# Performance work log

Measured on AMD Instinct MI355X. Metric: run time of the kernel, lower is better.

## Reference

```python
import jax, jax.numpy as jnp
import numpy as np

TOKENS, HIDDEN, FFN = 4096, 4096, 14336
SCALE = 0.02  # keep activations in a sane range


def setup_inputs() -> dict:
    key = jax.random.key(0)
    k1, k2, k3, k4 = jax.random.split(key, 4)
    x = jax.random.normal(k1, (TOKENS, HIDDEN), dtype=jnp.float32)
    expert_w1 = jax.random.normal(k2, (FFN, HIDDEN), dtype=jnp.float32) * SCALE
    expert_v1 = jax.random.normal(k3, (FFN, HIDDEN), dtype=jnp.float32) * SCALE
    expert_w2 = jax.random.normal(k4, (FFN, HIDDEN), dtype=jnp.float32) * SCALE
    return {"x": x, "expert_w1": expert_w1, "expert_v1": expert_v1, "expert_w2": expert_w2}


def reference(x, expert_w1, expert_v1, expert_w2):
    # gate/up projections: [T, H] @ [H, F] -> [T, F]
    gate = jnp.einsum('th,fh->tf', x, expert_w1)
    up = jnp.einsum('th,fh->tf', x, expert_v1)
    inter = jax.nn.silu(gate) * up            # fused SwiGLU intermediate [T, F]
    down = jnp.einsum('tf,fh->th', inter, expert_w2)  # [T, H]
    return down
```

## Files before the change

kernel.cpp:

```cpp
#include <hip/hip_runtime.h>
#include <hip/hip_bf16.h>
#include <stdint.h>

#define TOKENS 4096
#define HIDDEN 4096
#define FFN    14336

typedef __attribute__((ext_vector_type(8))) short bf16x8;
typedef __attribute__((ext_vector_type(4))) float f32x4;
typedef __attribute__((ext_vector_type(8))) unsigned short u16x8;

typedef __attribute__((address_space(3))) void lds_void_t;
typedef const __attribute__((address_space(1))) void gbl_void_t;

static __device__ __forceinline__ unsigned short f2b(float f) {
  union { float f; unsigned int u; } v; v.f = f;
  unsigned int u = v.u;
  return (unsigned short)((u + 0x7FFFu + ((u >> 16) & 1u)) >> 16);
}
static __device__ __forceinline__ float b2f(unsigned short b) {
  union { unsigned int u; float f; } v; v.u = ((unsigned int)b) << 16;
  return v.f;
}

__global__ void cvt_kernel(const float* __restrict__ in, unsigned short* __restrict__ out, long n) {
  long idx = (long)blockIdx.x * blockDim.x + threadIdx.x;
  long stride = (long)gridDim.x * blockDim.x;
  for (long i = idx * 4; i < n; i += stride * 4) {
    const float4 v = *reinterpret_cast<const float4*>(in + i);
    ushort4 o;
    o.x = f2b(v.x); o.y = f2b(v.y); o.z = f2b(v.z); o.w = f2b(v.w);
    *reinterpret_cast<ushort4*>(out + i) = o;
  }
}

__global__ void transpose_cvt_kernel(const float* __restrict__ in, unsigned short* __restrict__ out) {
  __shared__ float tile[64][65];
  const int f0 = blockIdx.x * 64;
  const int h0 = blockIdx.y * 64;
  const int t = threadIdx.x;
  const int rcol = (t & 15) * 4;
  const int rrow = t >> 4;
#pragma unroll
  for (int it = 0; it < 4; ++it) {
    int r = rrow + it * 16;
    const float4 v = *reinterpret_cast<const float4*>(in + (long)(f0 + r) * HIDDEN + h0 + rcol);
    tile[r][rcol] = v.x; tile[r][rcol + 1] = v.y; tile[r][rcol + 2] = v.z; tile[r][rcol + 3] = v.w;
  }
  __syncthreads();
  const int wrow = t >> 2;
  const int wc = (t & 3) * 16;
  u16x8 lo, hi;
#pragma unroll
  for (int j = 0; j < 8; ++j) lo[j] = f2b(tile[wc + j][wrow]);
#pragma unroll
  for (int j = 0; j < 8; ++j) hi[j] = f2b(tile[wc + 8 + j][wrow]);
  u16x8* dst = reinterpret_cast<u16x8*>(out + (long)(h0 + wrow) * FFN + f0 + wc);
  dst[0] = lo; dst[1] = hi;
}

#define MFMA16(a, b, c) __builtin_amdgcn_mfma_f32_16x16x32_bf16((a), (b), (c), 0, 0, 0)
#define SBAR()  __builtin_amdgcn_s_barrier()
#define SCHED0() __builtin_amdgcn_sched_barrier(0)

__global__ __launch_bounds__(512, 2)
void gateup256b_kernel(const unsigned short* __restrict__ X,
                       const unsigned short* __restrict__ W1,
                       const unsigned short* __restrict__ V1,
                       unsigned short* __restrict__ Inter) {
  __shared__ unsigned short sh[65536];
  const int tid = threadIdx.x, lane = tid & 63, wid = tid >> 6;
  const int wm = wid >> 2, wn = wid & 3;
  const int bm = blockIdx.x & 15;
  const int bn = blockIdx.x >> 4;
  const int sr = tid >> 3;
  const int scb = (((tid & 7) ^ (sr & 7)) << 4);
  const int l15 = lane & 15;
  const int cb0 = (((lane >> 4) * 16) ^ ((lane & 7) << 4));
  const int cb1 = ((64 + (lane >> 4) * 16) ^ ((lane & 7) << 4));

  const unsigned short* Ap = X  + (long)(bm * 256) * HIDDEN;
  const unsigned short* Wp = W1 + (long)(bn * 128) * HIDDEN;
  const unsigned short* Vp = V1 + (long)(bn * 128) * HIDDEN;

  f32x4 acc[8][4] = {};

  auto STAGE = [&](int kind, int h, int buf, int t) {
    const unsigned short* src;
    if (kind == 0) src = Ap + (long)(h * 128 + sr) * HIDDEN + t * 64 + (scb >> 1);
    else           src = (h ? Vp : Wp) + (long)sr * HIDDEN + t * 64 + (scb >> 1);
    unsigned short* dst = sh + buf * 32768 + kind * 16384 + h * 8192 + tid * 8;
    __builtin_amdgcn_global_load_lds((gbl_void_t*)src, (lds_void_t*)dst, 16, 0, 0);
    __builtin_amdgcn_global_load_lds((gbl_void_t*)(src + 64L * HIDDEN), (lds_void_t*)(dst + 4096), 16, 0, 0);
  };
  auto LDA8 = [&](bf16x8* a, int buf, int cb) {
    const char* base = (const char*)sh + buf * 65536 + wm * 16384 + l15 * 128 + cb;
#pragma unroll
    for (int m = 0; m < 8; ++m) a[m] = *(const bf16x8*)(base + m * 2048);
  };
  auto LDB2 = [&](bf16x8* b, int buf, int cb, int np) {
    const char* base = (const char*)sh + buf * 65536 + 32768 + (wn >> 1) * 16384 +
                       ((wn & 1) * 64 + l15) * 128 + cb;
    b[2 * np]     = *(const bf16x8*)(base + (2 * np) * 2048);
    b[2 * np + 1] = *(const bf16x8*)(base + (2 * np + 1) * 2048);
  };

  STAGE(0, 0, 0, 0); STAGE(0, 1, 0, 0); STAGE(1, 0, 0, 0); STAGE(1, 1, 0, 0);

  bf16x8 a[8], b[4];
  const int NT = HIDDEN / 64;
  for (int t = 0; t < NT; ++t) {
    const int cur = t & 1, nxt = cur ^ 1;
    const bool pre = (t + 1 < NT);
    if (pre) { STAGE(1, 0, nxt, t + 1); STAGE(1, 1, nxt, t + 1);
               asm volatile("s_waitcnt vmcnt(4)" ::: "memory"); }
    else     { asm volatile("s_waitcnt vmcnt(0)" ::: "memory"); }
    SBAR(); SCHED0();
    LDA8(a, cur, cb0); LDB2(b, cur, cb0, 0);
    __builtin_amdgcn_s_setprio(1);
#pragma unroll
    for (int m = 0; m < 8; ++m) {
      acc[m][0] = MFMA16(a[m], b[0], acc[m][0]);
      acc[m][1] = MFMA16(a[m], b[1], acc[m][1]);
    }
    __builtin_amdgcn_s_setprio(0);
    SCHED0(); SBAR();
    LDB2(b, cur, cb0, 1);
    if (pre) { STAGE(0, 0, nxt, t + 1); STAGE(0, 1, nxt, t + 1); }
    SCHED0(); SBAR();
    __builtin_amdgcn_s_setprio(1);
#pragma unroll
    for (int m = 0; m < 8; ++m) {
      acc[m][2] = MFMA16(a[m], b[2], acc[m][2]);
      acc[m][3] = MFMA16(a[m], b[3], acc[m][3]);
    }
    __builtin_amdgcn_s_setprio(0);
    SCHED0(); SBAR();
    LDA8(a, cur, cb1); LDB2(b, cur, cb1, 0);
    SCHED0(); SBAR();
    __builtin_amdgcn_s_setprio(1);
#pragma unroll
    for (int m = 0; m < 8; ++m) {
      acc[m][0] = MFMA16(a[m], b[0], acc[m][0]);
      acc[m][1] = MFMA16(a[m], b[1], acc[m][1]);
    }
    __builtin_amdgcn_s_setprio(0);
    SCHED0(); SBAR();
    LDB2(b, cur, cb1, 1);
    SCHED0(); SBAR();
    __builtin_amdgcn_s_setprio(1);
#pragma unroll
    for (int m = 0; m < 8; ++m) {
      acc[m][2] = MFMA16(a[m], b[2], acc[m][2]);
      acc[m][3] = MFMA16(a[m], b[3], acc[m][3]);
    }
    __builtin_amdgcn_s_setprio(0);
    SCHED0(); SBAR();
  }
  __syncthreads();
  if (wn >= 2) {
#pragma unroll
    for (int m = 0; m < 8; ++m)
#pragma unroll
      for (int n = 0; n < 4; ++n) {
        ushort4 p;
        p.x = f2b(acc[m][n][0]); p.y = f2b(acc[m][n][1]);
        p.z = f2b(acc[m][n][2]); p.w = f2b(acc[m][n][3]);
        const int idx = ((((wm * 2 + (wn & 1)) * 8 + m) * 4 + n) * 64 + lane) * 4;
        *reinterpret_cast<ushort4*>(&sh[idx]) = p;
      }
  }
  __syncthreads();
  if (wn < 2) {
    const int r0 = (lane >> 4) * 4;
#pragma unroll
    for (int m = 0; m < 8; ++m)
#pragma unroll
      for (int n = 0; n < 4; ++n) {
        const int idx = ((((wm * 2 + wn) * 8 + m) * 4 + n) * 64 + lane) * 4;
        const ushort4 p = *reinterpret_cast<const ushort4*>(&sh[idx]);
        const float uu[4] = { b2f(p.x), b2f(p.y), b2f(p.z), b2f(p.w) };
        const int row = bm * 256 + wm * 128 + m * 16 + r0;
        const int col = bn * 128 + wn * 64 + n * 16 + l15;
#pragma unroll
        for (int r = 0; r < 4; ++r) {
          const float g = acc[m][n][r];
          const float s = g / (1.0f + __expf(-g));
          Inter[(long)(row + r) * FFN + col] = f2b(s * uu[r]);
        }
      }
  }
}

__global__ __launch_bounds__(512, 2)
void down256_kernel(const unsigned short* __restrict__ Inter,
                    const unsigned short* __restrict__ W2t,
                    float* __restrict__ Out) {
  __shared__ unsigned short sh[65536];
  const int tid = threadIdx.x, lane = tid & 63, wid = tid >> 6;
  const int wm = wid >> 2, wn = wid & 3;
  const int bm = blockIdx.x & 15;
  const int bn = blockIdx.x >> 4;
  const int sr = tid >> 3;
  const int scb = (((tid & 7) ^ (sr & 7)) << 4);
  const int l15 = lane & 15;
  const int cb0 = (((lane >> 4) * 16) ^ ((lane & 7) << 4));
  const int cb1 = ((64 + (lane >> 4) * 16) ^ ((lane & 7) << 4));

  const unsigned short* Ap = Inter + (long)(bm * 256) * FFN;
  const unsigned short* Bp = W2t + (long)(bn * 256) * FFN;

  f32x4 acc[8][4] = {};

  auto STAGE = [&](int kind, int h, int buf, int t) {
    const unsigned short* src = (kind ? Bp : Ap) + (long)(h * 128 + sr) * FFN + t * 64 + (scb >> 1);
    unsigned short* dst = sh + buf * 32768 + kind * 16384 + h * 8192 + tid * 8;
    __builtin_amdgcn_global_load_lds((gbl_void_t*)src, (lds_void_t*)dst, 16, 0, 0);
    __builtin_amdgcn_global_load_lds((gbl_void_t*)(src + 64L * FFN), (lds_void_t*)(dst + 4096), 16, 0, 0);
  };
  auto LDA8 = [&](bf16x8* a, int buf, int cb) {
    const char* base = (const char*)sh + buf * 65536 + wm * 16384 + l15 * 128 + cb;
#pragma unroll
    for (int m = 0; m < 8; ++m) a[m] = *(const bf16x8*)(base + m * 2048);
  };
  auto LDB2 = [&](bf16x8* b, int buf, int cb, int np) {
    const char* base = (const char*)sh + buf * 65536 + 32768 + (wn >> 1) * 16384 +
                       ((wn & 1) * 64 + l15) * 128 + cb;
    b[2 * np]     = *(const bf16x8*)(base + (2 * np) * 2048);
    b[2 * np + 1] = *(const bf16x8*)(base + (2 * np + 1) * 2048);
  };

  STAGE(0, 0, 0, 0); STAGE(0, 1, 0, 0); STAGE(1, 0, 0, 0); STAGE(1, 1, 0, 0);

  bf16x8 a[8], b[4];
  const int NT = FFN / 64;
  for (int t = 0; t < NT; ++t) {
    const int cur = t & 1, nxt = cur ^ 1;
    const bool pre = (t + 1 < NT);
    if (pre) { STAGE(1, 0, nxt, t + 1); STAGE(1, 1, nxt, t + 1);
               asm volatile("s_waitcnt vmcnt(4)" ::: "memory"); }
    else     { asm volatile("s_waitcnt vmcnt(0)" ::: "memory"); }
    SBAR(); SCHED0();
    LDA8(a, cur, cb0); LDB2(b, cur, cb0, 0);
    __builtin_amdgcn_s_setprio(1);
#pragma unroll
    for (int m = 0; m < 8; ++m) {
      acc[m][0] = MFMA16(a[m], b[0], acc[m][0]);
      acc[m][1] = MFMA16(a[m], b[1], acc[m][1]);
    }
    __builtin_amdgcn_s_setprio(0);
    SCHED0(); SBAR();
    LDB2(b, cur, cb0, 1);
    if (pre) { STAGE(0, 0, nxt, t + 1); STAGE(0, 1, nxt, t + 1); }
    SCHED0(); SBAR();
    __builtin_amdgcn_s_setprio(1);
#pragma unroll
    for (int m = 0; m < 8; ++m) {
      acc[m][2] = MFMA16(a[m], b[2], acc[m][2]);
      acc[m][3] = MFMA16(a[m], b[3], acc[m][3]);
    }
    __builtin_amdgcn_s_setprio(0);
    SCHED0(); SBAR();
    LDA8(a, cur, cb1); LDB2(b, cur, cb1, 0);
    SCHED0(); SBAR();
    __builtin_amdgcn_s_setprio(1);
#pragma unroll
    for (int m = 0; m < 8; ++m) {
      acc[m][0] = MFMA16(a[m], b[0], acc[m][0]);
      acc[m][1] = MFMA16(a[m], b[1], acc[m][1]);
    }
    __builtin_amdgcn_s_setprio(0);
    SCHED0(); SBAR();
    LDB2(b, cur, cb1, 1);
    SCHED0(); SBAR();
    __builtin_amdgcn_s_setprio(1);
#pragma unroll
    for (int m = 0; m < 8; ++m) {
      acc[m][2] = MFMA16(a[m], b[2], acc[m][2]);
      acc[m][3] = MFMA16(a[m], b[3], acc[m][3]);
    }
    __builtin_amdgcn_s_setprio(0);
    SCHED0(); SBAR();
  }
  const int r0 = (lane >> 4) * 4;
#pragma unroll
  for (int m = 0; m < 8; ++m)
#pragma unroll
    for (int n = 0; n < 4; ++n)
#pragma unroll
      for (int r = 0; r < 4; ++r) {
        const int row = bm * 256 + wm * 128 + m * 16 + r0 + r;
        const int col = bn * 256 + wn * 64 + n * 16 + l15;
        Out[(long)row * HIDDEN + col] = acc[m][n][r];
      }
}

__device__ __forceinline__ void stage_tile_128(const unsigned short* __restrict__ g, long ldk,
                                               unsigned short* lds, int wave, int lane) {
#pragma unroll
  for (int it = 0; it < 2; ++it) {
    const int row = (it * 4 + wave) * 16 + (lane >> 2);
    const int kcol = (lane & 3) * 8;
    const unsigned short* src = g + (long)row * ldk + kcol;
    unsigned short* dst = lds + row * 32 + kcol;
    __builtin_amdgcn_global_load_lds((gbl_void_t*)src, (lds_void_t*)dst, 16, 0, 0);
  }
}

__global__ __launch_bounds__(256, 2)
void down_nt_kernel(const unsigned short* __restrict__ Inter,
                    const float* __restrict__ W2,
                    float* __restrict__ Out) {
  __shared__ unsigned short As[128 * 32];
  __shared__ unsigned short Bs[128 * 32];
  const int t = threadIdx.x;
  const int lane = t & 63;
  const int wave = t >> 6;
  const int bm = blockIdx.x & 31;
  const int bn = blockIdx.x >> 5;
  const int wm = (wave >> 1) * 64;
  const int wn = (wave & 1) * 64;
  const unsigned short* gA = Inter + (long)(bm * 128) * FFN;

  f32x4 acc[4][4] = {};
  const int fr = lane & 15;
  const int kg = (lane >> 4) * 8;
  const int p = lane & 15;
  const int h0 = wave * 32 + (lane >> 4) * 8;
  const float* gB = W2 + bn * 128 + h0;

  for (int kt = 0; kt < FFN; kt += 32) {
    __syncthreads();
    stage_tile_128(gA + kt, FFN, As, wave, lane);
    const float* r0p = gB + (long)(kt + 2 * p) * HIDDEN;
    const float* r1p = r0p + HIDDEN;
    const float4 a0 = *reinterpret_cast<const float4*>(r0p);
    const float4 a1 = *reinterpret_cast<const float4*>(r0p + 4);
    const float4 b0 = *reinterpret_cast<const float4*>(r1p);
    const float4 b1 = *reinterpret_cast<const float4*>(r1p + 4);
    unsigned short lo[8], hi[8];
    lo[0] = f2b(a0.x); lo[1] = f2b(a0.y); lo[2] = f2b(a0.z); lo[3] = f2b(a0.w);
    lo[4] = f2b(a1.x); lo[5] = f2b(a1.y); lo[6] = f2b(a1.z); lo[7] = f2b(a1.w);
    hi[0] = f2b(b0.x); hi[1] = f2b(b0.y); hi[2] = f2b(b0.z); hi[3] = f2b(b0.w);
    hi[4] = f2b(b1.x); hi[5] = f2b(b1.y); hi[6] = f2b(b1.z); hi[7] = f2b(b1.w);
#pragma unroll
    for (int j = 0; j < 8; ++j) {
      const unsigned int pack = (unsigned int)lo[j] | ((unsigned int)hi[j] << 16);
      *reinterpret_cast<unsigned int*>(&Bs[(h0 + j) * 32 + 2 * p]) = pack;
    }
    __syncthreads();
    bf16x8 a[4], b[4];
#pragma unroll
    for (int m = 0; m < 4; ++m)
      a[m] = *reinterpret_cast<const bf16x8*>(&As[(wm + m * 16 + fr) * 32 + kg]);
#pragma unroll
    for (int n = 0; n < 4; ++n)
      b[n] = *reinterpret_cast<const bf16x8*>(&Bs[(wn + n * 16 + fr) * 32 + kg]);
#pragma unroll
    for (int m = 0; m < 4; ++m)
#pragma unroll
      for (int n = 0; n < 4; ++n)
        acc[m][n] = MFMA16(a[m], b[n], acc[m][n]);
  }
  const int r0 = (lane >> 4) * 4;
#pragma unroll
  for (int m = 0; m < 4; ++m)
#pragma unroll
    for (int n = 0; n < 4; ++n)
#pragma unroll
      for (int r = 0; r < 4; ++r) {
        const int row = bm * 128 + wm + m * 16 + r0 + r;
        const int col = bn * 128 + wn + n * 16 + fr;
        Out[(long)row * HIDDEN + col] = acc[m][n][r];
      }
}

extern "C" void kernel_launch(void* const* d_in, const int* in_sizes, int n_in,
                              void* d_out, int out_size, void* d_ws, size_t ws_size,
                              hipStream_t stream) {
  const float* x  = (const float*)d_in[0];
  const float* w1 = (const float*)d_in[1];
  const float* v1 = (const float*)d_in[2];
  const float* w2 = (const float*)d_in[3];
  float* out = (float*)d_out;

  const size_t REQ_SMALL = 385875968UL;
  const size_t REQ_FULL  = 503316480UL;
  if (ws_size < REQ_SMALL) return;
  const bool full = (ws_size >= REQ_FULL);
  char* ws = (char*)d_ws;
  unsigned short* xb     = (unsigned short*)(ws);
  unsigned short* w1b    = (unsigned short*)(ws + 33554432L);
  unsigned short* v1b    = (unsigned short*)(ws + 150994944L);
  unsigned short* interb = (unsigned short*)(ws + 268435456L);
  unsigned short* w2tb   = (unsigned short*)(ws + 385875968L);

  hipLaunchKernelGGL(cvt_kernel, dim3(2048), dim3(256), 0, stream, x,  xb,  (long)TOKENS * HIDDEN);
  hipLaunchKernelGGL(cvt_kernel, dim3(2048), dim3(256), 0, stream, w1, w1b, (long)FFN * HIDDEN);
  hipLaunchKernelGGL(cvt_kernel, dim3(2048), dim3(256), 0, stream, v1, v1b, (long)FFN * HIDDEN);
  if (full)
    hipLaunchKernelGGL(transpose_cvt_kernel, dim3(FFN / 64, HIDDEN / 64), dim3(256), 0, stream, w2, w2tb);
  hipLaunchKernelGGL(gateup256b_kernel, dim3((TOKENS / 256) * (FFN / 128)), dim3(512), 0, stream,
                     xb, w1b, v1b, interb);
  if (full)
    hipLaunchKernelGGL(down256_kernel, dim3((TOKENS / 256) * (HIDDEN / 256)), dim3(512), 0, stream,
                       interb, w2tb, out);
  else
    hipLaunchKernelGGL(down_nt_kernel, dim3((TOKENS / 128) * (HIDDEN / 128)), dim3(256), 0, stream,
                       interb, w2, out);
}
```

Baseline: 1.475 ms.

## Split gate/up into two 256x256 GEMMs with SwiGLU fused into gate epilogue

Adds a templated 256x256-tile bf16 GEMM kernel whose epilogue can write bf16, write fp32, or apply SiLU(gate)*up by reading a stored up tensor. When the workspace is large enough, the fused gate/up kernel is replaced by two GEMM launches: the up projection writes a bf16 buffer, then the gate projection consumes it in its epilogue. The down projection now uses the same template, and the fp32-W2 fallback path is removed, so a larger minimum workspace is required. The aim is a uniform, simpler main loop per GEMM, at the cost of an extra round trip of the full T x F up intermediate through memory.

```diff
diff --git a/kernel.cpp b/kernel.cpp
--- a/kernel.cpp
+++ b/kernel.cpp
@@ -62,6 +62,120 @@
 #define MFMA16(a, b, c) __builtin_amdgcn_mfma_f32_16x16x32_bf16((a), (b), (c), 0, 0, 0)
 #define SBAR()  __builtin_amdgcn_s_barrier()
 #define SCHED0() __builtin_amdgcn_sched_barrier(0)
+
+template <int LDK, int NT, int LDN, int EPI>
+__global__ __launch_bounds__(512, 2)
+void gemm256_kernel(const unsigned short* __restrict__ A,
+                    const unsigned short* __restrict__ B,
+                    void* __restrict__ OutV,
+                    const unsigned short* __restrict__ Up) {
+  __shared__ unsigned short sh[65536];
+  const int tid = threadIdx.x, lane = tid & 63, wid = tid >> 6;
+  const int wm = wid >> 2, wn = wid & 3;
+  const int bm = blockIdx.x & 15;
+  const int bn = blockIdx.x >> 4;
+  const int sr = tid >> 3;
+  const int scb = (((tid & 7) ^ (sr & 7)) << 4);
+  const int l15 = lane & 15;
+  const int cb0 = (((lane >> 4) * 16) ^ ((lane & 7) << 4));
+  const int cb1 = ((64 + (lane >> 4) * 16) ^ ((lane & 7) << 4));
+
+  const unsigned short* Ap = A + (long)(bm * 256) * LDK;
+  const unsigned short* Bp = B + (long)(bn * 256) * LDK;
+
+  f32x4 acc[8][4] = {};
+
+  auto STAGE = [&](int kind, int h, int buf, int t) {
+    const unsigned short* src = (kind ? Bp : Ap) + (long)(h * 128 + sr) * LDK + t * 64 + (scb >> 1);
+    unsigned short* dst = sh + buf * 32768 + kind * 16384 + h * 8192 + tid * 8;
+    __builtin_amdgcn_global_load_lds((gbl_void_t*)src, (lds_void_t*)dst, 16, 0, 0);
+    __builtin_amdgcn_global_load_lds((gbl_void_t*)(src + 64L * LDK), (lds_void_t*)(dst + 4096), 16, 0, 0);
+  };
+  auto LDA8 = [&](bf16x8* a, int buf, int cb) {
+    const char* base = (const char*)sh + buf * 65536 + wm * 16384 + l15 * 128 + cb;
+#pragma unroll
+    for (int m = 0; m < 8; ++m) a[m] = *(const bf16x8*)(base + m * 2048);
+  };
+  auto LDB2 = [&](bf16x8* b, int buf, int cb, int np) {
+    const char* base = (const char*)sh + buf * 65536 + 32768 + (wn >> 1) * 16384 +
+                       ((wn & 1) * 64 + l15) * 128 + cb;
+    b[2 * np]     = *(const bf16x8*)(base + (2 * np) * 2048);
+    b[2 * np + 1] = *(const bf16x8*)(base + (2 * np + 1) * 2048);
+  };
+
+  STAGE(0, 0, 0, 0); STAGE(0, 1, 0, 0); STAGE(1, 0, 0, 0); STAGE(1, 1, 0, 0);
+
+  bf16x8 a[8], b[4];
+  for (int t = 0; t < NT; ++t) {
+    const int cur = t & 1, nxt = cur ^ 1;
+    const bool pre = (t + 1 < NT);
+    if (pre) { STAGE(1, 0, nxt, t + 1); STAGE(1, 1, nxt, t + 1);
+               asm volatile("s_waitcnt vmcnt(4)" ::: "memory"); }
+    else     { asm volatile("s_waitcnt vmcnt(0)" ::: "memory"); }
+    SBAR(); SCHED0();
+    LDA8(a, cur, cb0); LDB2(b, cur, cb0, 0);
+    __builtin_amdgcn_s_setprio(1);
+#pragma unroll
+    for (int m = 0; m < 8; ++m) {
+      acc[m][0] = MFMA16(a[m], b[0], acc[m][0]);
+      acc[m][1] = MFMA16(a[m], b[1], acc[m][1]);
+    }
+    __builtin_amdgcn_s_setprio(0);
+    SCHED0(); SBAR();
+    LDB2(b, cur, cb0, 1);
+    if (pre) { STAGE(0, 0, nxt, t + 1); STAGE(0, 1, nxt, t + 1); }
+    SCHED0(); SBAR();
+    __builtin_amdgcn_s_setprio(1);
+#pragma unroll
+    for (int m = 0; m < 8; ++m) {
+      acc[m][2] = MFMA16(a[m], b[2], acc[m][2]);
+      acc[m][3] = MFMA16(a[m], b[3], acc[m][3]);
+    }
+    __builtin_amdgcn_s_setprio(0);
+    SCHED0(); SBAR();
+    LDA8(a, cur, cb1); LDB2(b, cur, cb1, 0);
+    SCHED0(); SBAR();
+    __builtin_amdgcn_s_setprio(1);
+#pragma unroll
+    for (int m = 0; m < 8; ++m) {
+      acc[m][0] = MFMA16(a[m], b[0], acc[m][0]);
+      acc[m][1] = MFMA16(a[m], b[1], acc[m][1]);
+    }
+    __builtin_amdgcn_s_setprio(0);
+    SCHED0(); SBAR();
+    LDB2(b, cur, cb1, 1);
+    SCHED0(); SBAR();
+    __builtin_amdgcn_s_setprio(1);
+#pragma unroll
+    for (int m = 0; m < 8; ++m) {
+      acc[m][2] = MFMA16(a[m], b[2], acc[m][2]);
+      acc[m][3] = MFMA16(a[m], b[3], acc[m][3]);
+    }
+    __builtin_amdgcn_s_setprio(0);
+    SCHED0(); SBAR();
+  }
+  const int r0 = (lane >> 4) * 4;
+#pragma unroll
+  for (int m = 0; m < 8; ++m)
+#pragma unroll
+    for (int n = 0; n < 4; ++n) {
+      const long rowb = bm * 256 + wm * 128 + m * 16 + r0;
+      const long col = bn * 256 + wn * 64 + n * 16 + l15;
+#pragma unroll
+      for (int r = 0; r < 4; ++r) {
+        if (EPI == 1) {
+          ((float*)OutV)[(rowb + r) * (long)LDN + col] = acc[m][n][r];
+        } else if (EPI == 0) {
+          ((unsigned short*)OutV)[(rowb + r) * (long)LDN + col] = f2b(acc[m][n][r]);
+        } else {
+          const float u = b2f(Up[(rowb + r) * (long)LDN + col]);
+          const float g = acc[m][n][r];
+          const float s = g / (1.0f + __expf(-g));
+          ((unsigned short*)OutV)[(rowb + r) * (long)LDN + col] = f2b(s * u);
+        }
+      }
+    }
+}
 
 __global__ __launch_bounds__(512, 2)
 void gateup256b_kernel(const unsigned short* __restrict__ X,
@@ -192,189 +306,6 @@
   }
 }
 
-__global__ __launch_bounds__(512, 2)
-void down256_kernel(const unsigned short* __restrict__ Inter,
-                    const unsigned short* __restrict__ W2t,
-                    float* __restrict__ Out) {
-  __shared__ unsigned short sh[65536];
-  const int tid = threadIdx.x, lane = tid & 63, wid = tid >> 6;
-  const int wm = wid >> 2, wn = wid & 3;
-  const int bm = blockIdx.x & 15;
-  const int bn = blockIdx.x >> 4;
-  const int sr = tid >> 3;
-  const int scb = (((tid & 7) ^ (sr & 7)) << 4);
-  const int l15 = lane & 15;
-  const int cb0 = (((lane >> 4) * 16) ^ ((lane & 7) << 4));
-  const int cb1 = ((64 + (lane >> 4) * 16) ^ ((lane & 7) << 4));
-
-  const unsigned short* Ap = Inter + (long)(bm * 256) * FFN;
-  const unsigned short* Bp = W2t + (long)(bn * 256) * FFN;
-
-  f32x4 acc[8][4] = {};
-
-  auto STAGE = [&](int kind, int h, int buf, int t) {
-    const unsigned short* src = (kind ? Bp : Ap) + (long)(h * 128 + sr) * FFN + t * 64 + (scb >> 1);
-    unsigned short* dst = sh + buf * 32768 + kind * 16384 + h * 8192 + tid * 8;
-    __builtin_amdgcn_global_load_lds((gbl_void_t*)src, (lds_void_t*)dst, 16, 0, 0);
-    __builtin_amdgcn_global_load_lds((gbl_void_t*)(src + 64L * FFN), (lds_void_t*)(dst + 4096), 16, 0, 0);
-  };
-  auto LDA8 = [&](bf16x8* a, int buf, int cb) {
-    const char* base = (const char*)sh + buf * 65536 + wm * 16384 + l15 * 128 + cb;
-#pragma unroll
-    for (int m = 0; m < 8; ++m) a[m] = *(const bf16x8*)(base + m * 2048);
-  };
-  auto LDB2 = [&](bf16x8* b, int buf, int cb, int np) {
-    const char* base = (const char*)sh + buf * 65536 + 32768 + (wn >> 1) * 16384 +
-                       ((wn & 1) * 64 + l15) * 128 + cb;
-    b[2 * np]     = *(const bf16x8*)(base + (2 * np) * 2048);
-    b[2 * np + 1] = *(const bf16x8*)(base + (2 * np + 1) * 2048);
-  };
-
-  STAGE(0, 0, 0, 0); STAGE(0, 1, 0, 0); STAGE(1, 0, 0, 0); STAGE(1, 1, 0, 0);
-
-  bf16x8 a[8], b[4];
-  const int NT = FFN / 64;
-  for (int t = 0; t < NT; ++t) {
-    const int cur = t & 1, nxt = cur ^ 1;
-    const bool pre = (t + 1 < NT);
-    if (pre) { STAGE(1, 0, nxt, t + 1); STAGE(1, 1, nxt, t + 1);
-               asm volatile("s_waitcnt vmcnt(4)" ::: "memory"); }
-    else     { asm volatile("s_waitcnt vmcnt(0)" ::: "memory"); }
-    SBAR(); SCHED0();
-    LDA8(a, cur, cb0); LDB2(b, cur, cb0, 0);
-    __builtin_amdgcn_s_setprio(1);
-#pragma unroll
-    for (int m = 0; m < 8; ++m) {
-      acc[m][0] = MFMA16(a[m], b[0], acc[m][0]);
-      acc[m][1] = MFMA16(a[m], b[1], acc[m][1]);
-    }
-    __builtin_amdgcn_s_setprio(0);
-    SCHED0(); SBAR();
-    LDB2(b, cur, cb0, 1);
-    if (pre) { STAGE(0, 0, nxt, t + 1); STAGE(0, 1, nxt, t + 1); }
-    SCHED0(); SBAR();
-    __builtin_amdgcn_s_setprio(1);
-#pragma unroll
-    for (int m = 0; m < 8; ++m) {
-      acc[m][2] = MFMA16(a[m], b[2], acc[m][2]);
-      acc[m][3] = MFMA16(a[m], b[3], acc[m][3]);
-    }
-    __builtin_amdgcn_s_setprio(0);
-    SCHED0(); SBAR();
-    LDA8(a, cur, cb1); LDB2(b, cur, cb1, 0);
-    SCHED0(); SBAR();
-    __builtin_amdgcn_s_setprio(1);
-#pragma unroll
-    for (int m = 0; m < 8; ++m) {
-      acc[m][0] = MFMA16(a[m], b[0], acc[m][0]);
-      acc[m][1] = MFMA16(a[m], b[1], acc[m][1]);
-    }
-    __builtin_amdgcn_s_setprio(0);
-    SCHED0(); SBAR();
-    LDB2(b, cur, cb1, 1);
-    SCHED0(); SBAR();
-    __builtin_amdgcn_s_setprio(1);
-#pragma unroll
-    for (int m = 0; m < 8; ++m) {
-      acc[m][2] = MFMA16(a[m], b[2], acc[m][2]);
-      acc[m][3] = MFMA16(a[m], b[3], acc[m][3]);
-    }
-    __builtin_amdgcn_s_setprio(0);
-    SCHED0(); SBAR();
-  }
-  const int r0 = (lane >> 4) * 4;
-#pragma unroll
-  for (int m = 0; m < 8; ++m)
-#pragma unroll
-    for (int n = 0; n < 4; ++n)
-#pragma unroll
-      for (int r = 0; r < 4; ++r) {
-        const int row = bm * 256 + wm * 128 + m * 16 + r0 + r;
-        const int col = bn * 256 + wn * 64 + n * 16 + l15;
-        Out[(long)row * HIDDEN + col] = acc[m][n][r];
-      }
-}
-
-__device__ __forceinline__ void stage_tile_128(const unsigned short* __restrict__ g, long ldk,
-                                               unsigned short* lds, int wave, int lane) {
-#pragma unroll
-  for (int it = 0; it < 2; ++it) {
-    const int row = (it * 4 + wave) * 16 + (lane >> 2);
-    const int kcol = (lane & 3) * 8;
-    const unsigned short* src = g + (long)row * ldk + kcol;
-    unsigned short* dst = lds + row * 32 + kcol;
-    __builtin_amdgcn_global_load_lds((gbl_void_t*)src, (lds_void_t*)dst, 16, 0, 0);
-  }
-}
-
-__global__ __launch_bounds__(256, 2)
-void down_nt_kernel(const unsigned short* __restrict__ Inter,
-                    const float* __restrict__ W2,
-                    float* __restrict__ Out) {
-  __shared__ unsigned short As[128 * 32];
-  __shared__ unsigned short Bs[128 * 32];
-  const int t = threadIdx.x;
-  const int lane = t & 63;
-  const int wave = t >> 6;
-  const int bm = blockIdx.x & 31;
-  const int bn = blockIdx.x >> 5;
-  const int wm = (wave >> 1) * 64;
-  const int wn = (wave & 1) * 64;
-  const unsigned short* gA = Inter + (long)(bm * 128) * FFN;
-
-  f32x4 acc[4][4] = {};
-  const int fr = lane & 15;
-  const int kg = (lane >> 4) * 8;
-  const int p = lane & 15;
-  const int h0 = wave * 32 + (lane >> 4) * 8;
-  const float* gB = W2 + bn * 128 + h0;
-
-  for (int kt = 0; kt < FFN; kt += 32) {
-    __syncthreads();
-    stage_tile_128(gA + kt, FFN, As, wave, lane);
-    const float* r0p = gB + (long)(kt + 2 * p) * HIDDEN;
-    const float* r1p = r0p + HIDDEN;
-    const float4 a0 = *reinterpret_cast<const float4*>(r0p);
-    const float4 a1 = *reinterpret_cast<const float4*>(r0p + 4);
-    const float4 b0 = *reinterpret_cast<const float4*>(r1p);
-    const float4 b1 = *reinterpret_cast<const float4*>(r1p + 4);
-    unsigned short lo[8], hi[8];
-    lo[0] = f2b(a0.x); lo[1] = f2b(a0.y); lo[2] = f2b(a0.z); lo[3] = f2b(a0.w);
-    lo[4] = f2b(a1.x); lo[5] = f2b(a1.y); lo[6] = f2b(a1.z); lo[7] = f2b(a1.w);
-    hi[0] = f2b(b0.x); hi[1] = f2b(b0.y); hi[2] = f2b(b0.z); hi[3] = f2b(b0.w);
-    hi[4] = f2b(b1.x); hi[5] = f2b(b1.y); hi[6] = f2b(b1.z); hi[7] = f2b(b1.w);
-#pragma unroll
-    for (int j = 0; j < 8; ++j) {
-      const unsigned int pack = (unsigned int)lo[j] | ((unsigned int)hi[j] << 16);
-      *reinterpret_cast<unsigned int*>(&Bs[(h0 + j) * 32 + 2 * p]) = pack;
-    }
-    __syncthreads();
-    bf16x8 a[4], b[4];
-#pragma unroll
-    for (int m = 0; m < 4; ++m)
-      a[m] = *reinterpret_cast<const bf16x8*>(&As[(wm + m * 16 + fr) * 32 + kg]);
-#pragma unroll
-    for (int n = 0; n < 4; ++n)
-      b[n] = *reinterpret_cast<const bf16x8*>(&Bs[(wn + n * 16 + fr) * 32 + kg]);
-#pragma unroll
-    for (int m = 0; m < 4; ++m)
-#pragma unroll
-      for (int n = 0; n < 4; ++n)
-        acc[m][n] = MFMA16(a[m], b[n], acc[m][n]);
-  }
-  const int r0 = (lane >> 4) * 4;
-#pragma unroll
-  for (int m = 0; m < 4; ++m)
-#pragma unroll
-    for (int n = 0; n < 4; ++n)
-#pragma unroll
-      for (int r = 0; r < 4; ++r) {
-        const int row = bm * 128 + wm + m * 16 + r0 + r;
-        const int col = bn * 128 + wn + n * 16 + fr;
-        Out[(long)row * HIDDEN + col] = acc[m][n][r];
-      }
-}
-
 extern "C" void kernel_launch(void* const* d_in, const int* in_sizes, int n_in,
                               void* d_out, int out_size, void* d_ws, size_t ws_size,
                               hipStream_t stream) {
@@ -384,28 +315,40 @@
   const float* w2 = (const float*)d_in[3];
   float* out = (float*)d_out;
 
-  const size_t REQ_SMALL = 385875968UL;
-  const size_t REQ_FULL  = 503316480UL;
-  if (ws_size < REQ_SMALL) return;
-  const bool full = (ws_size >= REQ_FULL);
+  const size_t REQ_SPLIT = 620756992UL;
+  const size_t REQ_FUSED = 503316480UL;
+  if (ws_size < REQ_FUSED) return;
   char* ws = (char*)d_ws;
-  unsigned short* xb     = (unsigned short*)(ws);
-  unsigned short* w1b    = (unsigned short*)(ws + 33554432L);
-  unsigned short* v1b    = (unsigned short*)(ws + 150994944L);
-  unsigned short* interb = (unsigned short*)(ws + 268435456L);
-  unsigned short* w2tb   = (unsigned short*)(ws + 385875968L);
+  unsigned short* xb  = (unsigned short*)(ws);
+  unsigned short* w1b = (unsigned short*)(ws + 33554432L);
+  unsigned short* v1b = (unsigned short*)(ws + 150994944L);
 
   hipLaunchKernelGGL(cvt_kernel, dim3(2048), dim3(256), 0, stream, x,  xb,  (long)TOKENS * HIDDEN);
   hipLaunchKernelGGL(cvt_kernel, dim3(2048), dim3(256), 0, stream, w1, w1b, (long)FFN * HIDDEN);
   hipLaunchKernelGGL(cvt_kernel, dim3(2048), dim3(256), 0, stream, v1, v1b, (long)FFN * HIDDEN);
-  if (full)
+
+  if (ws_size >= REQ_SPLIT) {
+    unsigned short* upb    = (unsigned short*)(ws + 268435456L);
+    unsigned short* interb = (unsigned short*)(ws + 385875968L);
+    unsigned short* w2tb   = (unsigned short*)(ws + 503316480L);
     hipLaunchKernelGGL(transpose_cvt_kernel, dim3(FFN / 64, HIDDEN / 64), dim3(256), 0, stream, w2, w2tb);
-  hipLaunchKernelGGL(gateup256b_kernel, dim3((TOKENS / 256) * (FFN / 128)), dim3(512), 0, stream,
-                     xb, w1b, v1b, interb);
-  if (full)
-    hipLaunchKernelGGL(down256_kernel, dim3((TOKENS / 256) * (HIDDEN / 256)), dim3(512), 0, stream,
-                       interb, w2tb, out);
-  else
-    hipLaunchKernelGGL(down_nt_kernel, dim3((TOKENS / 128) * (HIDDEN / 128)), dim3(256), 0, stream,
-                       interb, w2, out);
-}
+    hipLaunchKernelGGL((gemm256_kernel<HIDDEN, HIDDEN / 64, FFN, 0>),
+                       dim3((TOKENS / 256) * (FFN / 256)), dim3(512), 0, stream,
+                       xb, v1b, (void*)upb, (const unsigned short*)nullptr);
+    hipLaunchKernelGGL((gemm256_kernel<HIDDEN, HIDDEN / 64, FFN, 2>),
+                       dim3((TOKENS / 256) * (FFN / 256)), dim3(512), 0, stream,
+                       xb, w1b, (void*)interb, upb);
+    hipLaunchKernelGGL((gemm256_kernel<FFN, FFN / 64, HIDDEN, 1>),
+                       dim3((TOKENS / 256) * (HIDDEN / 256)), dim3(512), 0, stream,
+                       interb, w2tb, (void*)out, (const unsigned short*)nullptr);
+  } else {
+    unsigned short* interb = (unsigned short*)(ws + 268435456L);
+    unsigned short* w2tb   = (unsigned short*)(ws + 385875968L);
+    hipLaunchKernelGGL(transpose_cvt_kernel, dim3(FFN / 64, HIDDEN / 64), dim3(256), 0, stream, w2, w2tb);
+    hipLaunchKernelGGL(gateup256b_kernel, dim3((TOKENS / 256) * (FFN / 128)), dim3(512), 0, stream,
+                       xb, w1b, v1b, interb);
+    hipLaunchKernelGGL((gemm256_kernel<FFN, FFN / 64, HIDDEN, 1>),
+                       dim3((TOKENS / 256) * (HIDDEN / 256)), dim3(512), 0, stream,
+                       interb, w2tb, (void*)out, (const unsigned short*)nullptr);
+  }
+}
```

Result: slower. 1.575 ms (+6.8%).
